# Optimization experiments

Hardware: AMD Instinct MI355X
Metric: run time of the kernel (lower is better)

Reference implementation:

```python
import jax, jax.numpy as jnp
import numpy as np

N_NODES = 50000
N_EDGES = 800000
F_IN = 64
H1 = 64
H2 = 64
OUT = 8
N_GRAPHS = 128


def gcn_conv(x, W, b, src, dst, n_nodes):
    """PyG GCNConv: sym-normalized aggregation with self-loops.
    out_i = sum_{j->i} d_j^{-1/2} d_i^{-1/2} (x_j W) + d_i^{-1} (x_i W) + b
    where d includes the self-loop (+1)."""
    h = x @ W  # [N, out]
    ones = jnp.ones((src.shape[0],), dtype=x.dtype)
    deg = jnp.zeros((n_nodes,), dtype=x.dtype).at[dst].add(ones) + 1.0  # +1 self-loop
    dinv_sqrt = jax.lax.rsqrt(deg)
    norm = dinv_sqrt[src] * dinv_sqrt[dst]  # [E]
    msgs = h[src] * norm[:, None]  # [E, out] -- dominant memory traffic
    agg = jax.ops.segment_sum(msgs, dst, num_segments=n_nodes)
    agg = agg + h * (1.0 / deg)[:, None]  # self-loop term (norm = 1/d_i)
    return agg + b


def setup_inputs() -> dict:
    key = jax.random.key(0)
    ks = jax.random.split(key, 10)
    x = jax.random.normal(ks[0], (N_NODES, F_IN), dtype=jnp.float32)
    src = jax.random.randint(ks[1], (N_EDGES,), 0, N_NODES, dtype=jnp.int32)
    dst = jax.random.randint(ks[2], (N_EDGES,), 0, N_NODES, dtype=jnp.int32)
    batch = jnp.sort(jax.random.randint(ks[3], (N_NODES,), 0, N_GRAPHS, dtype=jnp.int32))
    s1 = 1.0 / np.sqrt(F_IN)
    s2 = 1.0 / np.sqrt(H1)
    s3 = 1.0 / np.sqrt(H2)
    W1 = jax.random.uniform(ks[4], (F_IN, H1), jnp.float32, -s1, s1)
    b1 = jnp.zeros((H1,), jnp.float32)
    W2 = jax.random.uniform(ks[5], (H1, H2), jnp.float32, -s2, s2)
    b2 = jnp.zeros((H2,), jnp.float32)
    Wfc = jax.random.uniform(ks[6], (H2, OUT), jnp.float32, -s3, s3)
    bfc = jax.random.uniform(ks[7], (OUT,), jnp.float32, -s3, s3)
    return {"x": x, "src": src, "dst": dst, "batch": batch,
            "W1": W1, "b1": b1, "W2": W2, "b2": b2, "Wfc": Wfc, "bfc": bfc}


def reference(x, src, dst, batch, W1, b1, W2, b2, Wfc, bfc):
    n = x.shape[0]
    h = jnp.tanh(gcn_conv(x, W1, b1, src, dst, n))  # dropout(p=0) is identity
    h = jnp.tanh(gcn_conv(h, W2, b2, src, dst, n))
    # global mean pool over graphs
    sums = jax.ops.segment_sum(h, batch, num_segments=N_GRAPHS)  # [G, H2]
    counts = jax.ops.segment_sum(jnp.ones((n,), h.dtype), batch, num_segments=N_GRAPHS)
    pooled = sums / jnp.maximum(counts, 1.0)[:, None]
    return pooled @ Wfc + bfc  # [G, OUT]
```

## Files before the change

kernel.cpp:

```cpp
#include <hip/hip_runtime.h>
#include <math.h>


#define TPB 256
#define NBIN 256
#define NBLK 256
#define MSZ  (NBIN*NBLK)
#define CAP  4608

__global__ __launch_bounds__(TPB) void k_hist_gemm(const int* __restrict__ dst, int E,
                                                   int* __restrict__ Gh, int binw,
                                                   const float* __restrict__ X,
                                                   const float* __restrict__ W,
                                                   float* __restrict__ Y, int N) {
    if (blockIdx.x < NBIN) {
        __shared__ int hist[NBIN];
        hist[threadIdx.x] = 0;
        __syncthreads();
        int chunk = (E + NBLK - 1) / NBLK;
        int start = blockIdx.x * chunk;
        int end = min(start + chunk, E);
        for (int e = start + threadIdx.x; e < end; e += TPB)
            atomicAdd(&hist[dst[e] / binw], 1);
        __syncthreads();
        Gh[threadIdx.x * NBLK + blockIdx.x] = hist[threadIdx.x];
        return;
    }
    __shared__ float4 Ws[64][16];
    for (int i = threadIdx.x; i < 64 * 16; i += TPB)
        Ws[i >> 4][i & 15] = ((const float4*)W)[i];
    __syncthreads();

    int row = (blockIdx.x - NBIN) * TPB + threadIdx.x;
    if (row >= N) return;
    float xr[64];
    const float4* xp = (const float4*)(X + (size_t)row * 64);
#pragma unroll
    for (int q = 0; q < 16; q++) {
        float4 t = xp[q];
        xr[4 * q + 0] = t.x; xr[4 * q + 1] = t.y;
        xr[4 * q + 2] = t.z; xr[4 * q + 3] = t.w;
    }
    float4 acc[16];
#pragma unroll
    for (int q = 0; q < 16; q++) acc[q] = make_float4(0.f, 0.f, 0.f, 0.f);
#pragma unroll
    for (int k = 0; k < 64; k++) {
        float xk = xr[k];
#pragma unroll
        for (int q = 0; q < 16; q++) {
            float4 w = Ws[k][q];
            acc[q].x += xk * w.x; acc[q].y += xk * w.y;
            acc[q].z += xk * w.z; acc[q].w += xk * w.w;
        }
    }
    float4* yp = (float4*)(Y + (size_t)row * 64);
#pragma unroll
    for (int q = 0; q < 16; q++) yp[q] = acc[q];
}

__global__ __launch_bounds__(1024) void k_scanA(const int* __restrict__ Gh,
                                                int* __restrict__ localex,
                                                int* __restrict__ bsum) {
    __shared__ int buf[1024];
    int i = blockIdx.x * 1024 + threadIdx.x;
    int v = Gh[i];
    buf[threadIdx.x] = v;
    __syncthreads();
#pragma unroll
    for (int off = 1; off < 1024; off <<= 1) {
        int t = (threadIdx.x >= off) ? buf[threadIdx.x - off] : 0;
        __syncthreads();
        buf[threadIdx.x] += t;
        __syncthreads();
    }
    localex[i] = buf[threadIdx.x] - v;
    if (threadIdx.x == 1023) bsum[blockIdx.x] = buf[1023];
}

__global__ __launch_bounds__(1024) void k_scanC(const int* __restrict__ localex,
                                                const int* __restrict__ bsum,
                                                int* __restrict__ Gbase,
                                                int* __restrict__ binptr, int E) {
    __shared__ int offs;
    if (threadIdx.x == 0) {
        int run = 0;
        for (int j = 0; j < (int)blockIdx.x; j++) run += bsum[j];
        offs = run;
    }
    __syncthreads();
    int i = blockIdx.x * 1024 + threadIdx.x;
    int r = localex[i] + offs;
    Gbase[i] = r;
    if ((i & (NBLK - 1)) == 0) binptr[i / NBLK] = r;
    if (i == 0) binptr[NBIN] = E;
}

__global__ __launch_bounds__(TPB) void k_binscatter(const int* __restrict__ src,
                                                    const int* __restrict__ dst,
                                                    const int* __restrict__ Gbase,
                                                    unsigned int* __restrict__ Ebin,
                                                    int E, int binw) {
    __shared__ int curs[NBIN];
    curs[threadIdx.x] = Gbase[threadIdx.x * NBLK + blockIdx.x];
    __syncthreads();
    int chunk = (E + NBLK - 1) / NBLK;
    int start = blockIdx.x * chunk;
    int end = min(start + chunk, E);
    for (int e = start + threadIdx.x; e < end; e += TPB) {
        int d = dst[e], s = src[e];
        int pos = atomicAdd(&curs[d / binw], 1);
        Ebin[pos] = ((unsigned)d << 16) | (unsigned)s;
    }
}

__global__ __launch_bounds__(1024) void k_binsort(const unsigned int* __restrict__ Ebin,
                                                  const int* __restrict__ binptr,
                                                  int* __restrict__ rowptr,
                                                  int* __restrict__ eidx,
                                                  float* __restrict__ ds,
                                                  int N, int E, int binw) {
    __shared__ unsigned int eLDS[CAP];
    __shared__ int outLDS[CAP];
    __shared__ int hist[NBIN];
    __shared__ int scanb[NBIN];
    __shared__ int curs[NBIN];

    int b = blockIdx.x;
    int base = binptr[b];
    int cntE = min(binptr[b + 1] - base, CAP);
    int nodeBase = b * binw;

    if (threadIdx.x < NBIN) hist[threadIdx.x] = 0;
    __syncthreads();

    for (int j = threadIdx.x; j < cntE; j += 1024) {
        unsigned int u = Ebin[base + j];
        eLDS[j] = u;
        atomicAdd(&hist[(int)(u >> 16) - nodeBase], 1);
    }
    __syncthreads();

    int v = 0;
    if (threadIdx.x < NBIN) { v = hist[threadIdx.x]; scanb[threadIdx.x] = v; }
    __syncthreads();
#pragma unroll
    for (int off = 1; off < NBIN; off <<= 1) {
        int t = (threadIdx.x < NBIN && threadIdx.x >= off) ? scanb[threadIdx.x - off] : 0;
        __syncthreads();
        if (threadIdx.x < NBIN) scanb[threadIdx.x] += t;
        __syncthreads();
    }
    if (threadIdx.x < NBIN) {
        int excl = scanb[threadIdx.x] - v;
        curs[threadIdx.x] = excl;
        int node = nodeBase + threadIdx.x;
        if (threadIdx.x < binw && node < N) {
            rowptr[node] = base + excl;
            ds[node] = rsqrtf((float)v + 1.0f);
        }
    }
    if (b == NBIN - 1 && threadIdx.x == 0) rowptr[N] = E;
    __syncthreads();

    for (int j = threadIdx.x; j < cntE; j += 1024) {
        unsigned int u = eLDS[j];
        int p = atomicAdd(&curs[(int)(u >> 16) - nodeBase], 1);
        outLDS[p] = (int)(u & 0xFFFFu);
    }
    __syncthreads();
    for (int j = threadIdx.x; j < cntE; j += 1024)
        eidx[base + j] = outLDS[j];
}

__global__ __launch_bounds__(TPB) void k_scale(float4* __restrict__ A,
                                               const float* __restrict__ ds, int N) {
    int i = blockIdx.x * TPB + threadIdx.x;
    if (i < N * 16) {
        float s = ds[i >> 4];
        float4 v = A[i];
        v.x *= s; v.y *= s; v.z *= s; v.w *= s;
        A[i] = v;
    }
}

__global__ __launch_bounds__(TPB) void k_agg4(const float4* __restrict__ Hp,
                                              float4* __restrict__ O,
                                              const int* __restrict__ rowptr,
                                              const int* __restrict__ eidx,
                                              const float* __restrict__ ds,
                                              const float* __restrict__ b, int N) {
    int wid = (blockIdx.x * TPB + threadIdx.x) >> 6;
    int lane = threadIdx.x & 63;
    if (wid >= N) return;
    int r = lane >> 4;
    int c = lane & 15;

    int lo = rowptr[wid], hi = rowptr[wid + 1];
    float4 a0 = make_float4(0.f, 0.f, 0.f, 0.f);
    float4 a1 = make_float4(0.f, 0.f, 0.f, 0.f);

    int base = lo;
    for (; base + 8 <= hi; base += 8) {
        int s0 = eidx[base + r], s1 = eidx[base + 4 + r];
        float4 v0 = Hp[(size_t)s0 * 16 + c];
        float4 v1 = Hp[(size_t)s1 * 16 + c];
        a0.x += v0.x; a0.y += v0.y; a0.z += v0.z; a0.w += v0.w;
        a1.x += v1.x; a1.y += v1.y; a1.z += v1.z; a1.w += v1.w;
    }
    if (base + 4 <= hi) {
        int s0 = eidx[base + r];
        float4 v0 = Hp[(size_t)s0 * 16 + c];
        a0.x += v0.x; a0.y += v0.y; a0.z += v0.z; a0.w += v0.w;
        base += 4;
    }
    int rem = hi - base;
    if (r < rem) {
        int s0 = eidx[base + r];
        float4 v0 = Hp[(size_t)s0 * 16 + c];
        a0.x += v0.x; a0.y += v0.y; a0.z += v0.z; a0.w += v0.w;
    }
    a0.x += a1.x; a0.y += a1.y; a0.z += a1.z; a0.w += a1.w;

    a0.x += __shfl_xor(a0.x, 16); a0.y += __shfl_xor(a0.y, 16);
    a0.z += __shfl_xor(a0.z, 16); a0.w += __shfl_xor(a0.w, 16);
    a0.x += __shfl_xor(a0.x, 32); a0.y += __shfl_xor(a0.y, 32);
    a0.z += __shfl_xor(a0.z, 32); a0.w += __shfl_xor(a0.w, 32);

    if (r == 0) {
        float4 self = Hp[(size_t)wid * 16 + c];
        float dsd = ds[wid];
        float4 bb = ((const float4*)b)[c];
        float4 o;
        o.x = tanhf((a0.x + self.x) * dsd + bb.x);
        o.y = tanhf((a0.y + self.y) * dsd + bb.y);
        o.z = tanhf((a0.z + self.z) * dsd + bb.z);
        o.w = tanhf((a0.w + self.w) * dsd + bb.w);
        O[(size_t)wid * 16 + c] = o;
    }
}

__global__ __launch_bounds__(TPB) void k_gemm64s(const float* __restrict__ X,
                                                 const float* __restrict__ W,
                                                 float* __restrict__ Y, int N,
                                                 const float* __restrict__ ds) {
    __shared__ float4 Ws[64][16];
    for (int i = threadIdx.x; i < 64 * 16; i += TPB)
        Ws[i >> 4][i & 15] = ((const float4*)W)[i];
    __syncthreads();

    int row = blockIdx.x * TPB + threadIdx.x;
    if (row >= N) return;
    float xr[64];
    const float4* xp = (const float4*)(X + (size_t)row * 64);
#pragma unroll
    for (int q = 0; q < 16; q++) {
        float4 t = xp[q];
        xr[4 * q + 0] = t.x; xr[4 * q + 1] = t.y;
        xr[4 * q + 2] = t.z; xr[4 * q + 3] = t.w;
    }
    float4 acc[16];
#pragma unroll
    for (int q = 0; q < 16; q++) acc[q] = make_float4(0.f, 0.f, 0.f, 0.f);
#pragma unroll
    for (int k = 0; k < 64; k++) {
        float xk = xr[k];
#pragma unroll
        for (int q = 0; q < 16; q++) {
            float4 w = Ws[k][q];
            acc[q].x += xk * w.x; acc[q].y += xk * w.y;
            acc[q].z += xk * w.z; acc[q].w += xk * w.w;
        }
    }
    float s = ds[row];
    float4* yp = (float4*)(Y + (size_t)row * 64);
#pragma unroll
    for (int q = 0; q < 16; q++) {
        acc[q].x *= s; acc[q].y *= s; acc[q].z *= s; acc[q].w *= s;
        yp[q] = acc[q];
    }
}

__global__ __launch_bounds__(TPB) void k_poolfc(const float* __restrict__ H,
                                                const int* __restrict__ batch,
                                                const float* __restrict__ Wfc,
                                                const float* __restrict__ bfc,
                                                float* __restrict__ out, int N) {
    int g = blockIdx.x;
    __shared__ int range[2];
    __shared__ float red[4][64];
    if (threadIdx.x == 0) {
        int lo = 0, hi = N;
        while (lo < hi) { int m = (lo + hi) >> 1; if (batch[m] < g) lo = m + 1; else hi = m; }
        range[0] = lo;
        hi = N;
        while (lo < hi) { int m = (lo + hi) >> 1; if (batch[m] < g + 1) lo = m + 1; else hi = m; }
        range[1] = lo;
    }
    __syncthreads();
    int lo = range[0], hi = range[1];
    int wid = threadIdx.x >> 6, lane = threadIdx.x & 63;

    float acc = 0.0f;
    for (int n = lo + wid; n < hi; n += 4) acc += H[(size_t)n * 64 + lane];
    red[wid][lane] = acc;
    __syncthreads();
    if (wid == 0) {
        float s = red[0][lane] + red[1][lane] + red[2][lane] + red[3][lane];
        float cgt = fmaxf((float)(hi - lo), 1.0f);
        red[0][lane] = s / cgt;
    }
    __syncthreads();
    if (threadIdx.x < 8) {
        int o = threadIdx.x;
        float accf = bfc[o];
#pragma unroll
        for (int f = 0; f < 64; f++) accf += red[0][f] * Wfc[f * 8 + o];
        out[g * 8 + o] = accf;
    }
}

extern "C" void kernel_launch(void* const* d_in, const int* in_sizes, int n_in,
                              void* d_out, int out_size, void* d_ws, size_t ws_size,
                              hipStream_t stream) {
    const float* x     = (const float*)d_in[0];
    const int*   src   = (const int*)d_in[1];
    const int*   dst   = (const int*)d_in[2];
    const int*   batch = (const int*)d_in[3];
    const float* W1    = (const float*)d_in[4];
    const float* b1    = (const float*)d_in[5];
    const float* W2    = (const float*)d_in[6];
    const float* b2    = (const float*)d_in[7];
    const float* Wfc   = (const float*)d_in[8];
    const float* bfc   = (const float*)d_in[9];
    float* out = (float*)d_out;

    const int N = in_sizes[0] / 64;
    const int E = in_sizes[1];
    const int G = out_size / 8;
    const int binw = (N + NBIN - 1) / NBIN;

    const size_t NB = (size_t)N * 64 * sizeof(float);
    char* ws = (char*)d_ws;
    size_t off = 0;
    float* A      = (float*)(ws + off); off += NB;
    float* B      = (float*)(ws + off); off += NB;
    unsigned int* Ebin = (unsigned int*)B;
    int*   eidx   = (int*)(ws + off);   off += (size_t)E * 4;
    int*   Gh     = (int*)(ws + off);   off += (size_t)MSZ * 4;
    int*   localx = (int*)(ws + off);   off += (size_t)MSZ * 4;
    int*   Gbase  = (int*)(ws + off);   off += (size_t)MSZ * 4;
    int*   binptr = (int*)(ws + off);   off += (size_t)(NBIN + 1) * 4;
    int*   bsum   = (int*)(ws + off);   off += 256;
    int*   rowptr = (int*)(ws + off);   off += (size_t)(N + 1) * 4;
    float* dsv    = (float*)(ws + off); off += (size_t)N * 4;

    const int gN = (N + TPB - 1) / TPB;
    const int gS = (N * 16 + TPB - 1) / TPB;
    const int gW = (N * 64 + TPB - 1) / TPB;

    k_hist_gemm<<<NBIN + gN, TPB, 0, stream>>>(dst, E, Gh, binw, x, W1, A, N);
    k_scanA<<<MSZ / 1024, 1024, 0, stream>>>(Gh, localx, bsum);
    k_scanC<<<MSZ / 1024, 1024, 0, stream>>>(localx, bsum, Gbase, binptr, E);
    k_binscatter<<<NBLK, TPB, 0, stream>>>(src, dst, Gbase, Ebin, E, binw);
    k_binsort<<<NBIN, 1024, 0, stream>>>(Ebin, binptr, rowptr, eidx, dsv, N, E, binw);
    k_scale<<<gS, TPB, 0, stream>>>((float4*)A, dsv, N);

    k_agg4<<<gW, TPB, 0, stream>>>((const float4*)A, (float4*)B, rowptr, eidx, dsv, b1, N);
    k_gemm64s<<<gN, TPB, 0, stream>>>(B, W2, A, N, dsv);
    k_agg4<<<gW, TPB, 0, stream>>>((const float4*)A, (float4*)B, rowptr, eidx, dsv, b2, N);
    k_poolfc<<<G, TPB, 0, stream>>>(B, batch, Wfc, bfc, out, N);
}
```

Before: 171.3 us.

## Store scaled node features in fp16 for gather aggregation and fuse scaling into binsort

The pre-scaled feature matrix gathered by the aggregation kernels is now stored as fp16, which halves the bytes read per edge gather. Each lane loads 8 halves and accumulates in fp32. The separate degree-scaling kernel is removed: binsort now scales the first-layer features and converts them to fp16 in the same pass, and the second-layer GEMM writes fp16 directly. This cuts random-gather memory traffic and one kernel launch, at the cost of reduced precision in the aggregated messages.

```diff
diff --git a/kernel.cpp b/kernel.cpp
--- a/kernel.cpp
+++ b/kernel.cpp
@@ -1,4 +1,5 @@
 #include <hip/hip_runtime.h>
+#include <hip/hip_fp16.h>
 #include <math.h>
 
 
@@ -7,6 +8,12 @@
 #define NBLK 256
 #define MSZ  (NBIN*NBLK)
 #define CAP  4608
+
+#define ADD8(a, v) do { const __half2* _h = (const __half2*)&(v);             \
+    float2 _f0 = __half22float2(_h[0]), _f1 = __half22float2(_h[1]);          \
+    float2 _f2 = __half22float2(_h[2]), _f3 = __half22float2(_h[3]);          \
+    a[0] += _f0.x; a[1] += _f0.y; a[2] += _f1.x; a[3] += _f1.y;               \
+    a[4] += _f2.x; a[5] += _f2.y; a[6] += _f3.x; a[7] += _f3.y; } while (0)
 
 __global__ __launch_bounds__(TPB) void k_hist_gemm(const int* __restrict__ dst, int E,
                                                    int* __restrict__ Gh, int binw,
@@ -119,6 +126,8 @@
                                                   int* __restrict__ rowptr,
                                                   int* __restrict__ eidx,
                                                   float* __restrict__ ds,
+                                                  const float* __restrict__ A,
+                                                  __half* __restrict__ Ah,
                                                   int N, int E, int binw) {
     __shared__ unsigned int eLDS[CAP];
     __shared__ int outLDS[CAP];
@@ -171,78 +180,87 @@
     __syncthreads();
     for (int j = threadIdx.x; j < cntE; j += 1024)
         eidx[base + j] = outLDS[j];
-}
-
-__global__ __launch_bounds__(TPB) void k_scale(float4* __restrict__ A,
-                                               const float* __restrict__ ds, int N) {
-    int i = blockIdx.x * TPB + threadIdx.x;
-    if (i < N * 16) {
-        float s = ds[i >> 4];
-        float4 v = A[i];
-        v.x *= s; v.y *= s; v.z *= s; v.w *= s;
-        A[i] = v;
-    }
-}
-
-__global__ __launch_bounds__(TPB) void k_agg4(const float4* __restrict__ Hp,
-                                              float4* __restrict__ O,
-                                              const int* __restrict__ rowptr,
-                                              const int* __restrict__ eidx,
-                                              const float* __restrict__ ds,
-                                              const float* __restrict__ b, int N) {
+
+    const float2* A2 = (const float2*)A;
+    __half2* Ah2 = (__half2*)Ah;
+    int total = binw * 32;
+    for (int j = threadIdx.x; j < total; j += 1024) {
+        int li = j >> 5;
+        int node = nodeBase + li;
+        if (node >= N) continue;
+        float s = rsqrtf((float)hist[li] + 1.0f);
+        int c2 = j & 31;
+        float2 t = A2[(size_t)node * 32 + c2];
+        Ah2[(size_t)node * 32 + c2] = __float22half2_rn(make_float2(t.x * s, t.y * s));
+    }
+}
+
+__global__ __launch_bounds__(TPB) void k_agg8h(const float4* __restrict__ Hp,
+                                               float4* __restrict__ O,
+                                               const int* __restrict__ rowptr,
+                                               const int* __restrict__ eidx,
+                                               const float* __restrict__ ds,
+                                               const float* __restrict__ b, int N) {
     int wid = (blockIdx.x * TPB + threadIdx.x) >> 6;
     int lane = threadIdx.x & 63;
     if (wid >= N) return;
-    int r = lane >> 4;
-    int c = lane & 15;
+    int r = lane >> 3;
+    int c = lane & 7;
 
     int lo = rowptr[wid], hi = rowptr[wid + 1];
-    float4 a0 = make_float4(0.f, 0.f, 0.f, 0.f);
-    float4 a1 = make_float4(0.f, 0.f, 0.f, 0.f);
+    float a[8] = {0.f, 0.f, 0.f, 0.f, 0.f, 0.f, 0.f, 0.f};
 
     int base = lo;
-    for (; base + 8 <= hi; base += 8) {
-        int s0 = eidx[base + r], s1 = eidx[base + 4 + r];
-        float4 v0 = Hp[(size_t)s0 * 16 + c];
-        float4 v1 = Hp[(size_t)s1 * 16 + c];
-        a0.x += v0.x; a0.y += v0.y; a0.z += v0.z; a0.w += v0.w;
-        a1.x += v1.x; a1.y += v1.y; a1.z += v1.z; a1.w += v1.w;
-    }
-    if (base + 4 <= hi) {
+    for (; base + 16 <= hi; base += 16) {
+        int s0 = eidx[base + r], s1 = eidx[base + 8 + r];
+        float4 v0 = Hp[(size_t)s0 * 8 + c];
+        float4 v1 = Hp[(size_t)s1 * 8 + c];
+        ADD8(a, v0);
+        ADD8(a, v1);
+    }
+    if (base + 8 <= hi) {
         int s0 = eidx[base + r];
-        float4 v0 = Hp[(size_t)s0 * 16 + c];
-        a0.x += v0.x; a0.y += v0.y; a0.z += v0.z; a0.w += v0.w;
-        base += 4;
+        float4 v0 = Hp[(size_t)s0 * 8 + c];
+        ADD8(a, v0);
+        base += 8;
     }
     int rem = hi - base;
     if (r < rem) {
         int s0 = eidx[base + r];
-        float4 v0 = Hp[(size_t)s0 * 16 + c];
-        a0.x += v0.x; a0.y += v0.y; a0.z += v0.z; a0.w += v0.w;
-    }
-    a0.x += a1.x; a0.y += a1.y; a0.z += a1.z; a0.w += a1.w;
-
-    a0.x += __shfl_xor(a0.x, 16); a0.y += __shfl_xor(a0.y, 16);
-    a0.z += __shfl_xor(a0.z, 16); a0.w += __shfl_xor(a0.w, 16);
-    a0.x += __shfl_xor(a0.x, 32); a0.y += __shfl_xor(a0.y, 32);
-    a0.z += __shfl_xor(a0.z, 32); a0.w += __shfl_xor(a0.w, 32);
+        float4 v0 = Hp[(size_t)s0 * 8 + c];
+        ADD8(a, v0);
+    }
+
+#pragma unroll
+    for (int j = 0; j < 8; j++) a[j] += __shfl_xor(a[j], 8);
+#pragma unroll
+    for (int j = 0; j < 8; j++) a[j] += __shfl_xor(a[j], 16);
+#pragma unroll
+    for (int j = 0; j < 8; j++) a[j] += __shfl_xor(a[j], 32);
 
     if (r == 0) {
-        float4 self = Hp[(size_t)wid * 16 + c];
+        float4 sv = Hp[(size_t)wid * 8 + c];
+        ADD8(a, sv);
         float dsd = ds[wid];
-        float4 bb = ((const float4*)b)[c];
-        float4 o;
-        o.x = tanhf((a0.x + self.x) * dsd + bb.x);
-        o.y = tanhf((a0.y + self.y) * dsd + bb.y);
-        o.z = tanhf((a0.z + self.z) * dsd + bb.z);
-        o.w = tanhf((a0.w + self.w) * dsd + bb.w);
-        O[(size_t)wid * 16 + c] = o;
-    }
-}
-
-__global__ __launch_bounds__(TPB) void k_gemm64s(const float* __restrict__ X,
+        float4 bb0 = ((const float4*)b)[c * 2];
+        float4 bb1 = ((const float4*)b)[c * 2 + 1];
+        float4 o0, o1;
+        o0.x = tanhf(a[0] * dsd + bb0.x);
+        o0.y = tanhf(a[1] * dsd + bb0.y);
+        o0.z = tanhf(a[2] * dsd + bb0.z);
+        o0.w = tanhf(a[3] * dsd + bb0.w);
+        o1.x = tanhf(a[4] * dsd + bb1.x);
+        o1.y = tanhf(a[5] * dsd + bb1.y);
+        o1.z = tanhf(a[6] * dsd + bb1.z);
+        o1.w = tanhf(a[7] * dsd + bb1.w);
+        O[(size_t)wid * 16 + c * 2] = o0;
+        O[(size_t)wid * 16 + c * 2 + 1] = o1;
+    }
+}
+
+__global__ __launch_bounds__(TPB) void k_gemm64h(const float* __restrict__ X,
                                                  const float* __restrict__ W,
-                                                 float* __restrict__ Y, int N,
+                                                 __half* __restrict__ Ah, int N,
                                                  const float* __restrict__ ds) {
     __shared__ float4 Ws[64][16];
     for (int i = threadIdx.x; i < 64 * 16; i += TPB)
@@ -273,11 +291,11 @@
         }
     }
     float s = ds[row];
-    float4* yp = (float4*)(Y + (size_t)row * 64);
+    __half2* yh = (__half2*)(Ah + (size_t)row * 64);
 #pragma unroll
     for (int q = 0; q < 16; q++) {
-        acc[q].x *= s; acc[q].y *= s; acc[q].z *= s; acc[q].w *= s;
-        yp[q] = acc[q];
+        yh[2 * q]     = __float22half2_rn(make_float2(acc[q].x * s, acc[q].y * s));
+        yh[2 * q + 1] = __float22half2_rn(make_float2(acc[q].z * s, acc[q].w * s));
     }
 }
 
@@ -346,6 +364,7 @@
     float* A      = (float*)(ws + off); off += NB;
     float* B      = (float*)(ws + off); off += NB;
     unsigned int* Ebin = (unsigned int*)B;
+    __half* Ah    = (__half*)(ws + off); off += NB / 2;
     int*   eidx   = (int*)(ws + off);   off += (size_t)E * 4;
     int*   Gh     = (int*)(ws + off);   off += (size_t)MSZ * 4;
     int*   localx = (int*)(ws + off);   off += (size_t)MSZ * 4;
@@ -356,18 +375,16 @@
     float* dsv    = (float*)(ws + off); off += (size_t)N * 4;
 
     const int gN = (N + TPB - 1) / TPB;
-    const int gS = (N * 16 + TPB - 1) / TPB;
     const int gW = (N * 64 + TPB - 1) / TPB;
 
     k_hist_gemm<<<NBIN + gN, TPB, 0, stream>>>(dst, E, Gh, binw, x, W1, A, N);
     k_scanA<<<MSZ / 1024, 1024, 0, stream>>>(Gh, localx, bsum);
     k_scanC<<<MSZ / 1024, 1024, 0, stream>>>(localx, bsum, Gbase, binptr, E);
     k_binscatter<<<NBLK, TPB, 0, stream>>>(src, dst, Gbase, Ebin, E, binw);
-    k_binsort<<<NBIN, 1024, 0, stream>>>(Ebin, binptr, rowptr, eidx, dsv, N, E, binw);
-    k_scale<<<gS, TPB, 0, stream>>>((float4*)A, dsv, N);
-
-    k_agg4<<<gW, TPB, 0, stream>>>((const float4*)A, (float4*)B, rowptr, eidx, dsv, b1, N);
-    k_gemm64s<<<gN, TPB, 0, stream>>>(B, W2, A, N, dsv);
-    k_agg4<<<gW, TPB, 0, stream>>>((const float4*)A, (float4*)B, rowptr, eidx, dsv, b2, N);
+    k_binsort<<<NBIN, 1024, 0, stream>>>(Ebin, binptr, rowptr, eidx, dsv, A, Ah, N, E, binw);
+
+    k_agg8h<<<gW, TPB, 0, stream>>>((const float4*)Ah, (float4*)B, rowptr, eidx, dsv, b1, N);
+    k_gemm64h<<<gN, TPB, 0, stream>>>(B, W2, Ah, N, dsv);
+    k_agg8h<<<gW, TPB, 0, stream>>>((const float4*)Ah, (float4*)B, rowptr, eidx, dsv, b2, N);
     k_poolfc<<<G, TPB, 0, stream>>>(B, batch, Wfc, bfc, out, N);
 }
```

Measured after the change: 155.6 us, median of 2. -9.2%, faster.
